# Kernel tuning notes

Hardware: AMD Instinct MI355X
Metric: run time of the kernel (lower is better)

## Reference

```python
import jax, jax.numpy as jnp
import numpy as np

EPS = 1e-8
NUM_LAYERS = 6


def setup_inputs() -> dict:
    key = jax.random.key(0)
    ks = jax.random.split(key, 8)
    N, Cin, Cout, S, H, W = 4, 256, 256, 512, 64, 64
    fan_in = Cin  # kaiming for 1x1 conv, leaky_relu a=0 -> gain sqrt(2)
    return {
        "x": jax.random.normal(ks[0], (N, Cin, H, W), dtype=jnp.float32),
        "y": jax.random.normal(ks[1], (N, S), dtype=jnp.float32),
        "ch_conv_w": jax.random.normal(ks[2], (Cout, Cin), dtype=jnp.float32) / np.sqrt(fan_in),
        "ch_conv_b": jnp.zeros((Cout,), dtype=jnp.float32),
        "affine_w": jax.random.normal(ks[3], (NUM_LAYERS, Cout, S), dtype=jnp.float32) / np.sqrt(S),
        "affine_b": jnp.zeros((NUM_LAYERS, Cout), dtype=jnp.float32),
        "mod_w": jax.random.normal(ks[4], (NUM_LAYERS, Cout, Cout), dtype=jnp.float32) * np.sqrt(2.0 / Cout),
    }


def _forward(x, y, ch_conv_w, ch_conv_b, affine_w, affine_b, mod_w):
    # 1x1 channel conv (with bias)
    x = jnp.einsum("oi,bihw->bohw", ch_conv_w, x) + ch_conv_b[None, :, None, None]
    x = jnp.repeat(jnp.repeat(x, 2, axis=2), 2, axis=3)
    # channel repeat_interleave(2) -> [N, 2C, H, W]
    x = jnp.repeat(x, 2, axis=1)

    C = x.shape[1] // 2
    for i in range(NUM_LAYERS):
        x1, x2 = x[:, :C], x[:, C:]
        # SpatialShift2d with default directions pads [1,1,1,1] (replicate) then
        # crops the identical region for every split -> exact identity.
        y1 = x1 + x2
        # g-branch: Conv2dMod(k=1) with per-sample style modulation + exact GELU
        s = jnp.einsum("cs,bs->bc", affine_w[i], y) + affine_b[i]  # [B, C]
        wmod = mod_w[i][None] * (s[:, :, None] + 1.0)              # [B, O, I] (style scales OUTPUT channel)
        d = jax.lax.rsqrt(jnp.sum(wmod * wmod, axis=2, keepdims=True) + EPS)
        wmod = wmod * d
        h = jnp.einsum("boi,bihw->bohw", wmod, y1)
        y2 = x2 + jax.nn.gelu(h, approximate=False)
        x = jnp.concatenate([y1, y2], axis=1)

    x1, x2 = x[:, :C], x[:, C:]
    return (x1 + x2) * 0.5


def reference(x, y, ch_conv_w, ch_conv_b, affine_w, affine_b, mod_w):
    return _forward(x, y, ch_conv_w, ch_conv_b, affine_w, affine_b, mod_w)
```

## Files before the change

kernel.cpp:

```cpp
#include <hip/hip_runtime.h>
#include <math.h>

#define NB 4
#define CC 256
#define SS 512
#define NL 6
#define SLOT_HW 65536
#define G_OFF_HW   (7*SLOT_HW)

typedef __attribute__((ext_vector_type(8))) short s16x8;
typedef __attribute__((ext_vector_type(4))) float f32x4;
typedef __attribute__((ext_vector_type(2))) float f32x2;

#define PIN(v) asm volatile("" :: "v"(v))

__device__ __forceinline__ unsigned short f2bf(float f) {
    unsigned u = __builtin_bit_cast(unsigned, f);
    u += 0x7FFFu + ((u >> 16) & 1u);
    return (unsigned short)(u >> 16);
}
__device__ __forceinline__ unsigned cvt_pk_bf16(float lo, float hi) {
    unsigned r;
    asm("v_cvt_pk_bf16_f32 %0, %1, %2" : "=v"(r) : "v"(lo), "v"(hi));
    return r;
}
__device__ __forceinline__ float gelu_fast(float x) {
    float u = x * (1.0f + 0.044715f * x * x);
    float e = __expf(-1.5957691216f * u);
    return x * __builtin_amdgcn_rcpf(1.0f + e);
}


__global__ __launch_bounds__(256) void prep_kernel(
    const float* __restrict__ y, const float* __restrict__ aw,
    const float* __restrict__ ab, const float* __restrict__ mw,
    const float* __restrict__ cw, unsigned short* __restrict__ wsBF)
{
    int w = threadIdx.x >> 6, lane = threadIdx.x & 63;
    float* gtab = (float*)(wsBF + G_OFF_HW);

    if (blockIdx.x < 448) {
        int row = blockIdx.x*4 + w;
        int sl  = row >> 8, m = row & 255;
        const float* src = (sl == 0) ? (cw + (size_t)m*CC)
                                     : (mw + ((size_t)(sl-1)*CC + m)*CC);
        unsigned short* dst = wsBF + (size_t)sl*SLOT_HW;
#pragma unroll
        for (int u = 0; u < 4; ++u) {
            int k = lane + 64*u;
            int f = (m >> 4)*8 + (k >> 5);
            int hw = f*512 + ((k >> 3) & 3)*128 + (m & 15)*8 + (k & 7);
            dst[hw] = f2bf(src[k]);
        }
        return;
    }

    int r  = (blockIdx.x - 448)*4 + w;
    int pl = r >> 8, po = r & 255;

    const float* awr = aw + (size_t)(pl*CC + po)*SS;
    float s[4] = {0.f, 0.f, 0.f, 0.f};
#pragma unroll
    for (int j = 0; j < 8; ++j) {
        int idx = lane + 64*j;
        float a = awr[idx];
#pragma unroll
        for (int b = 0; b < 4; ++b) s[b] += a * y[(size_t)b*SS + idx];
    }
    const float* mwr = mw + ((size_t)pl*CC + po)*CC;
    float qs = 0.f;
#pragma unroll
    for (int u = 0; u < 4; ++u) { float v = mwr[lane + 64*u]; qs += v*v; }
#pragma unroll
    for (int off = 32; off; off >>= 1) {
#pragma unroll
        for (int b = 0; b < 4; ++b) s[b] += __shfl_xor(s[b], off);
        qs += __shfl_xor(qs, off);
    }
    float abv = ab[pl*CC + po];
    if (lane < 4) {
        float t = s[lane] + abv + 1.0f;
        gtab[pl*1024 + lane*256 + po] = t * (1.0f / sqrtf(t*t*qs + 1e-8f));
    }
}

#define BFRAGL(buf, kq, nt, kcl) \
    (lds + (buf)*16384 + ((((kq)*2 + (nt))*2 + (kcl)))*1024)

__global__ __launch_bounds__(512, 4) void fused_kernel(
    const float* __restrict__ x, const float* __restrict__ cb,
    const unsigned short* __restrict__ wsBF, float* __restrict__ out)
{
    __shared__ __align__(16) unsigned char lds[69632];
    float* xS = (float*)(lds + 32768);
    float* S2 = (float*)(lds + 32768);
    const float* gtab = (const float*)(wsBF + G_OFF_HW);

    const int tid  = threadIdx.x;
    const int lane = tid & 63;
    const int w    = tid >> 6;
    const int l15  = lane & 15;
    const int q    = lane >> 4;

    const int bswz  = blockIdx.x & 7;
    const int b     = bswz >> 1;
    const int half  = bswz & 1;
    const int strip = blockIdx.x >> 3;
    const int n0    = strip * 64 + half * 32;

    float y1[2][2][4], y2[2][2][4];
    f32x4 acc[2][2];

#pragma unroll
    for (int t = 0; t < 2; ++t)
#pragma unroll
        for (int s = 0; s < 2; ++s) acc[t][s] = 0;

    float4 xr[4];
#pragma unroll
    for (int p = 0; p < 4; ++p) {
        int row = (tid >> 3) + 64*p, c4 = (tid & 7) * 4;
        xr[p] = *(const float4*)&x[((size_t)(b*CC + row))*4096 + n0 + c4];
    }
    s16x8 aS[8][2];
#pragma unroll
    for (int p = 0; p < 4; ++p)
#pragma unroll
    for (int t = 0; t < 2; ++t)
        aS[p][t] = *(const s16x8*)(wsBF + (size_t)(((2*w+t)*8 + p)*512) + lane*8);

#pragma unroll
    for (int p = 0; p < 4; ++p) {
        int row = (tid >> 3) + 64*p, c4 = (tid & 7) * 4;
        *(float4*)&xS[row*36 + c4] = xr[p];
    }
    __syncthreads();
    {
        int n = tid & 31, k0 = (tid >> 5) * 16;
        int nt = n >> 4, n15 = n & 15;
#pragma unroll
        for (int j = 0; j < 4; ++j) {
            int k = k0 + 4*j;
            float v0 = xS[(k+0)*36 + n], v1 = xS[(k+1)*36 + n];
            float v2 = xS[(k+2)*36 + n], v3 = xS[(k+3)*36 + n];
            uint2 hv; hv.x = cvt_pk_bf16(v0, v1); hv.y = cvt_pk_bf16(v2, v3);
            int kq = k >> 6, kcl = (k >> 5) & 1, qq = (k >> 3) & 3, jb = k & 7;
            *(uint2*)(BFRAGL(0,kq,nt,kcl) + (16*qq + n15)*16 + jb*2) = hv;
        }
    }
#pragma unroll
    for (int p = 0; p < 4; ++p) { PIN(aS[p][0]); PIN(aS[p][1]); }
    __syncthreads();
    {
        const unsigned short* slot = wsBF;
        __builtin_amdgcn_s_setprio(1);
#pragma unroll
        for (int step = 0; step < 8; ++step) {
            if (step < 4) {
#pragma unroll
                for (int t = 0; t < 2; ++t)
                    aS[step+4][t] = *(const s16x8*)(slot + (size_t)(((2*w+t)*8 + step+4)*512) + lane*8);
            }
            int kq = step >> 1, kcl = step & 1;
#pragma unroll
            for (int s = 0; s < 2; ++s) {
                s16x8 bh = *(const s16x8*)(BFRAGL(0,kq,s,kcl) + lane*16);
#pragma unroll
                for (int t = 0; t < 2; ++t)
                    acc[t][s] = __builtin_amdgcn_mfma_f32_16x16x32_bf16(aS[step][t], bh, acc[t][s], 0, 0, 0);
            }
        }
        __builtin_amdgcn_s_setprio(0);
    }

#pragma unroll
    for (int t = 0; t < 2; ++t)
#pragma unroll
    for (int s = 0; s < 2; ++s)
#pragma unroll
    for (int r = 0; r < 4; ++r) {
        int m  = 32*w + 16*t + 4*q + r;
        int nl = 16*s + l15;
        S2[m*33 + nl] = acc[t][s][r] + cb[m];
    }
    __syncthreads();
#pragma unroll
    for (int t = 0; t < 2; ++t)
#pragma unroll
    for (int s = 0; s < 2; ++s)
#pragma unroll
    for (int r = 0; r < 4; ++r) {
        int c  = 32*w + 16*t + 4*q + r;
        int nl = 16*s + l15;
        float a  = S2[(c >> 1)*33 + nl];
        float bb = S2[(128 + (c >> 1))*33 + nl];
        y1[t][s][r] = a + bb;
        y2[t][s][r] = bb;
    }

    for (int l = 0; l < NL; ++l) {
        const int buf = l & 1;
        const unsigned short* slot = wsBF + (size_t)(1 + l)*SLOT_HW;
#pragma unroll
        for (int t = 0; t < 2; ++t)
#pragma unroll
            for (int s = 0; s < 2; ++s) acc[t][s] = 0;

#pragma unroll
        for (int p = 0; p < 4; ++p)
#pragma unroll
        for (int t = 0; t < 2; ++t)
            aS[p][t] = *(const s16x8*)(slot + (size_t)(((2*w+t)*8 + p)*512) + lane*8);
        float4 gv[2];
#pragma unroll
        for (int t = 0; t < 2; ++t)
            gv[t] = *(const float4*)&gtab[l*1024 + b*256 + 32*w + 16*t + 4*q];

        {
            int kq = w >> 1, kcl = w & 1, jb = 4*(q & 1);
#pragma unroll
            for (int t = 0; t < 2; ++t) {
                int qq = 2*t + (q >> 1);
#pragma unroll
                for (int s = 0; s < 2; ++s) {
                    uint2 hv;
                    hv.x = cvt_pk_bf16(y1[t][s][0], y1[t][s][1]);
                    hv.y = cvt_pk_bf16(y1[t][s][2], y1[t][s][3]);
                    *(uint2*)(BFRAGL(buf,kq,s,kcl) + (16*qq + l15)*16 + jb*2) = hv;
                }
            }
        }
#pragma unroll
        for (int p = 0; p < 4; ++p) { PIN(aS[p][0]); PIN(aS[p][1]); }
        __syncthreads();
        __builtin_amdgcn_s_setprio(1);
#pragma unroll
        for (int step = 0; step < 8; ++step) {
            if (step < 4) {
#pragma unroll
                for (int t = 0; t < 2; ++t)
                    aS[step+4][t] = *(const s16x8*)(slot + (size_t)(((2*w+t)*8 + step+4)*512) + lane*8);
            }
            int kq = step >> 1, kcl = step & 1;
#pragma unroll
            for (int s = 0; s < 2; ++s) {
                s16x8 bh = *(const s16x8*)(BFRAGL(buf,kq,s,kcl) + lane*16);
#pragma unroll
                for (int t = 0; t < 2; ++t)
                    acc[t][s] = __builtin_amdgcn_mfma_f32_16x16x32_bf16(aS[step][t], bh, acc[t][s], 0, 0, 0);
            }
        }
        __builtin_amdgcn_s_setprio(0);

        if (l < NL - 1) {
#pragma unroll
            for (int t = 0; t < 2; ++t)
#pragma unroll
            for (int s = 0; s < 2; ++s)
#pragma unroll
            for (int r = 0; r < 4; ++r) {
                y2[t][s][r] += gelu_fast(acc[t][s][r] * gv[t][r]);
                y1[t][s][r] += y2[t][s][r];
            }
        } else {
#pragma unroll
            for (int t = 0; t < 2; ++t)
#pragma unroll
            for (int s = 0; s < 2; ++s)
#pragma unroll
            for (int r = 0; r < 4; ++r) {
                float yf = y2[t][s][r] + gelu_fast(acc[t][s][r] * gv[t][r]);
                float v  = 0.5f*(y1[t][s][r] + yf);
                int ch  = 32*w + 16*t + 4*q + r;
                int wpx = half*32 + 16*s + l15;
                f32x2 vv = {v, v};
                size_t base = (((size_t)(b*CC + ch)*128 + 2*strip))*128 + 2*wpx;
                __builtin_nontemporal_store(vv, (f32x2*)&out[base]);
                __builtin_nontemporal_store(vv, (f32x2*)&out[base + 128]);
            }
        }
    }
}

extern "C" void kernel_launch(void* const* d_in, const int* in_sizes, int n_in,
                              void* d_out, int out_size, void* d_ws, size_t ws_size,
                              hipStream_t stream) {
    const float* x  = (const float*)d_in[0];
    const float* y  = (const float*)d_in[1];
    const float* cw = (const float*)d_in[2];
    const float* cb = (const float*)d_in[3];
    const float* aw = (const float*)d_in[4];
    const float* ab = (const float*)d_in[5];
    const float* mw = (const float*)d_in[6];
    float* out = (float*)d_out;

    unsigned short* wsBF = (unsigned short*)d_ws;

    prep_kernel<<<832, 256, 0, stream>>>(y, aw, ab, mw, cw, wsBF);
    fused_kernel<<<512, 512, 0, stream>>>(x, cb, wsBF, out);
}
```

Measured before the change: 120.2 us.

## Halve per-block pixel tile to 16 and double grid for higher occupancy

Each block now handles 16 pixels instead of 32, so the grid doubles to 1024 blocks and LDS drops to 40KB. The launch-bounds occupancy hint rises from 4 to 8. The A-fragment prefetch becomes a 3-deep ring buffer of weight registers, which cuts register pressure. The gtab load moves after the MFMA loop, and the bias loads are vectorised. The aim is more resident waves to hide the latency of the global weight loads. In exchange, every weight fragment is loaded twice as often across the grid, and each B fragment read feeds only two MFMAs.

```diff
diff --git a/kernel.cpp b/kernel.cpp
--- a/kernel.cpp
+++ b/kernel.cpp
@@ -84,16 +84,16 @@
     }
 }
 
-#define BFRAGL(buf, kq, nt, kcl) \
-    (lds + (buf)*16384 + ((((kq)*2 + (nt))*2 + (kcl)))*1024)
-
-__global__ __launch_bounds__(512, 4) void fused_kernel(
+#define BFRAG16(buf, kq, kcl) \
+    (lds + (buf)*8192 + ((kq)*2 + (kcl))*1024)
+
+__global__ __launch_bounds__(512, 8) void fused_kernel(
     const float* __restrict__ x, const float* __restrict__ cb,
     const unsigned short* __restrict__ wsBF, float* __restrict__ out)
 {
-    __shared__ __align__(16) unsigned char lds[69632];
-    float* xS = (float*)(lds + 32768);
-    float* S2 = (float*)(lds + 32768);
+    __shared__ __align__(16) unsigned char lds[40960];
+    float* xS = (float*)(lds + 16384);
+    float* S2 = (float*)(lds + 16384);
     const float* gtab = (const float*)(wsBF + G_OFF_HW);
 
     const int tid  = threadIdx.x;
@@ -102,177 +102,149 @@
     const int l15  = lane & 15;
     const int q    = lane >> 4;
 
-    const int bswz  = blockIdx.x & 7;
-    const int b     = bswz >> 1;
-    const int half  = bswz & 1;
-    const int strip = blockIdx.x >> 3;
-    const int n0    = strip * 64 + half * 32;
-
-    float y1[2][2][4], y2[2][2][4];
-    f32x4 acc[2][2];
-
+    const int b       = blockIdx.x & 3;
+    const int quarter = (blockIdx.x >> 2) & 3;
+    const int strip   = blockIdx.x >> 4;
+    const int n0      = strip*64 + quarter*16;
+
+    float y1[2][4], y2[2][4];
+    f32x4 acc[2];
+    acc[0] = 0; acc[1] = 0;
+
+    float4 xr[2];
+#pragma unroll
+    for (int p = 0; p < 2; ++p) {
+        int row = (tid >> 2) + 128*p, c4 = (tid & 3) * 4;
+        xr[p] = *(const float4*)&x[((size_t)(b*CC + row))*4096 + n0 + c4];
+    }
+    s16x8 aA[3][2];
+#pragma unroll
+    for (int p = 0; p < 2; ++p)
 #pragma unroll
     for (int t = 0; t < 2; ++t)
-#pragma unroll
-        for (int s = 0; s < 2; ++s) acc[t][s] = 0;
-
-    float4 xr[4];
-#pragma unroll
-    for (int p = 0; p < 4; ++p) {
-        int row = (tid >> 3) + 64*p, c4 = (tid & 7) * 4;
-        xr[p] = *(const float4*)&x[((size_t)(b*CC + row))*4096 + n0 + c4];
-    }
-    s16x8 aS[8][2];
-#pragma unroll
-    for (int p = 0; p < 4; ++p)
-#pragma unroll
-    for (int t = 0; t < 2; ++t)
-        aS[p][t] = *(const s16x8*)(wsBF + (size_t)(((2*w+t)*8 + p)*512) + lane*8);
-
-#pragma unroll
-    for (int p = 0; p < 4; ++p) {
-        int row = (tid >> 3) + 64*p, c4 = (tid & 7) * 4;
-        *(float4*)&xS[row*36 + c4] = xr[p];
+        aA[p][t] = *(const s16x8*)(wsBF + (size_t)(((2*w+t)*8 + p)*512) + lane*8);
+
+#pragma unroll
+    for (int p = 0; p < 2; ++p) {
+        int row = (tid >> 2) + 128*p, c4 = (tid & 3) * 4;
+        *(float4*)&xS[row*24 + c4] = xr[p];
     }
     __syncthreads();
     {
-        int n = tid & 31, k0 = (tid >> 5) * 16;
-        int nt = n >> 4, n15 = n & 15;
-#pragma unroll
-        for (int j = 0; j < 4; ++j) {
-            int k = k0 + 4*j;
-            float v0 = xS[(k+0)*36 + n], v1 = xS[(k+1)*36 + n];
-            float v2 = xS[(k+2)*36 + n], v3 = xS[(k+3)*36 + n];
-            uint2 hv; hv.x = cvt_pk_bf16(v0, v1); hv.y = cvt_pk_bf16(v2, v3);
-            int kq = k >> 6, kcl = (k >> 5) & 1, qq = (k >> 3) & 3, jb = k & 7;
-            *(uint2*)(BFRAGL(0,kq,nt,kcl) + (16*qq + n15)*16 + jb*2) = hv;
-        }
-    }
-#pragma unroll
-    for (int p = 0; p < 4; ++p) { PIN(aS[p][0]); PIN(aS[p][1]); }
+        int n = tid & 15, k0 = (tid >> 4) * 8;
+        float v[8];
+#pragma unroll
+        for (int i = 0; i < 8; ++i) v[i] = xS[(k0+i)*24 + n];
+        uint4 hv;
+        hv.x = cvt_pk_bf16(v[0], v[1]); hv.y = cvt_pk_bf16(v[2], v[3]);
+        hv.z = cvt_pk_bf16(v[4], v[5]); hv.w = cvt_pk_bf16(v[6], v[7]);
+        int kq = k0 >> 6, kcl = (k0 >> 5) & 1, qq = (k0 >> 3) & 3;
+        *(uint4*)(BFRAG16(0,kq,kcl) + (16*qq + n)*16) = hv;
+    }
+    PIN(aA[0][0]); PIN(aA[0][1]); PIN(aA[1][0]); PIN(aA[1][1]);
     __syncthreads();
     {
         const unsigned short* slot = wsBF;
         __builtin_amdgcn_s_setprio(1);
 #pragma unroll
         for (int step = 0; step < 8; ++step) {
-            if (step < 4) {
+            if (step < 6) {
 #pragma unroll
                 for (int t = 0; t < 2; ++t)
-                    aS[step+4][t] = *(const s16x8*)(slot + (size_t)(((2*w+t)*8 + step+4)*512) + lane*8);
-            }
-            int kq = step >> 1, kcl = step & 1;
-#pragma unroll
-            for (int s = 0; s < 2; ++s) {
-                s16x8 bh = *(const s16x8*)(BFRAGL(0,kq,s,kcl) + lane*16);
-#pragma unroll
-                for (int t = 0; t < 2; ++t)
-                    acc[t][s] = __builtin_amdgcn_mfma_f32_16x16x32_bf16(aS[step][t], bh, acc[t][s], 0, 0, 0);
-            }
+                    aA[(step+2)%3][t] = *(const s16x8*)(slot + (size_t)(((2*w+t)*8 + step+2)*512) + lane*8);
+            }
+            s16x8 bh = *(const s16x8*)(BFRAG16(0, step>>1, step&1) + lane*16);
+            acc[0] = __builtin_amdgcn_mfma_f32_16x16x32_bf16(aA[step%3][0], bh, acc[0], 0, 0, 0);
+            acc[1] = __builtin_amdgcn_mfma_f32_16x16x32_bf16(aA[step%3][1], bh, acc[1], 0, 0, 0);
         }
         __builtin_amdgcn_s_setprio(0);
     }
 
+    {
+        float4 cbv[2];
+#pragma unroll
+        for (int t = 0; t < 2; ++t)
+            cbv[t] = *(const float4*)&cb[32*w + 16*t + 4*q];
+#pragma unroll
+        for (int t = 0; t < 2; ++t)
+#pragma unroll
+        for (int r = 0; r < 4; ++r) {
+            int m = 32*w + 16*t + 4*q + r;
+            S2[m*18 + l15] = acc[t][r] + cbv[t][r];
+        }
+    }
+    __syncthreads();
 #pragma unroll
     for (int t = 0; t < 2; ++t)
 #pragma unroll
-    for (int s = 0; s < 2; ++s)
-#pragma unroll
     for (int r = 0; r < 4; ++r) {
-        int m  = 32*w + 16*t + 4*q + r;
-        int nl = 16*s + l15;
-        S2[m*33 + nl] = acc[t][s][r] + cb[m];
-    }
-    __syncthreads();
-#pragma unroll
-    for (int t = 0; t < 2; ++t)
-#pragma unroll
-    for (int s = 0; s < 2; ++s)
-#pragma unroll
-    for (int r = 0; r < 4; ++r) {
-        int c  = 32*w + 16*t + 4*q + r;
-        int nl = 16*s + l15;
-        float a  = S2[(c >> 1)*33 + nl];
-        float bb = S2[(128 + (c >> 1))*33 + nl];
-        y1[t][s][r] = a + bb;
-        y2[t][s][r] = bb;
+        int c = 32*w + 16*t + 4*q + r, h = c >> 1;
+        float a  = S2[h*18 + l15];
+        float bb = S2[(128 + h)*18 + l15];
+        y1[t][r] = a + bb;
+        y2[t][r] = bb;
     }
 
     for (int l = 0; l < NL; ++l) {
         const int buf = l & 1;
         const unsigned short* slot = wsBF + (size_t)(1 + l)*SLOT_HW;
-#pragma unroll
-        for (int t = 0; t < 2; ++t)
-#pragma unroll
-            for (int s = 0; s < 2; ++s) acc[t][s] = 0;
-
-#pragma unroll
-        for (int p = 0; p < 4; ++p)
-#pragma unroll
-        for (int t = 0; t < 2; ++t)
-            aS[p][t] = *(const s16x8*)(slot + (size_t)(((2*w+t)*8 + p)*512) + lane*8);
-        float4 gv[2];
-#pragma unroll
-        for (int t = 0; t < 2; ++t)
-            gv[t] = *(const float4*)&gtab[l*1024 + b*256 + 32*w + 16*t + 4*q];
+        acc[0] = 0; acc[1] = 0;
+
+#pragma unroll
+        for (int p = 0; p < 2; ++p)
+#pragma unroll
+        for (int t = 0; t < 2; ++t)
+            aA[p][t] = *(const s16x8*)(slot + (size_t)(((2*w+t)*8 + p)*512) + lane*8);
 
         {
             int kq = w >> 1, kcl = w & 1, jb = 4*(q & 1);
 #pragma unroll
             for (int t = 0; t < 2; ++t) {
                 int qq = 2*t + (q >> 1);
-#pragma unroll
-                for (int s = 0; s < 2; ++s) {
-                    uint2 hv;
-                    hv.x = cvt_pk_bf16(y1[t][s][0], y1[t][s][1]);
-                    hv.y = cvt_pk_bf16(y1[t][s][2], y1[t][s][3]);
-                    *(uint2*)(BFRAGL(buf,kq,s,kcl) + (16*qq + l15)*16 + jb*2) = hv;
-                }
-            }
-        }
-#pragma unroll
-        for (int p = 0; p < 4; ++p) { PIN(aS[p][0]); PIN(aS[p][1]); }
+                uint2 hv;
+                hv.x = cvt_pk_bf16(y1[t][0], y1[t][1]);
+                hv.y = cvt_pk_bf16(y1[t][2], y1[t][3]);
+                *(uint2*)(BFRAG16(buf,kq,kcl) + (16*qq + l15)*16 + jb*2) = hv;
+            }
+        }
+        PIN(aA[0][0]); PIN(aA[0][1]); PIN(aA[1][0]); PIN(aA[1][1]);
         __syncthreads();
         __builtin_amdgcn_s_setprio(1);
 #pragma unroll
         for (int step = 0; step < 8; ++step) {
-            if (step < 4) {
+            if (step < 6) {
 #pragma unroll
                 for (int t = 0; t < 2; ++t)
-                    aS[step+4][t] = *(const s16x8*)(slot + (size_t)(((2*w+t)*8 + step+4)*512) + lane*8);
-            }
-            int kq = step >> 1, kcl = step & 1;
-#pragma unroll
-            for (int s = 0; s < 2; ++s) {
-                s16x8 bh = *(const s16x8*)(BFRAGL(buf,kq,s,kcl) + lane*16);
-#pragma unroll
-                for (int t = 0; t < 2; ++t)
-                    acc[t][s] = __builtin_amdgcn_mfma_f32_16x16x32_bf16(aS[step][t], bh, acc[t][s], 0, 0, 0);
-            }
+                    aA[(step+2)%3][t] = *(const s16x8*)(slot + (size_t)(((2*w+t)*8 + step+2)*512) + lane*8);
+            }
+            s16x8 bh = *(const s16x8*)(BFRAG16(buf, step>>1, step&1) + lane*16);
+            acc[0] = __builtin_amdgcn_mfma_f32_16x16x32_bf16(aA[step%3][0], bh, acc[0], 0, 0, 0);
+            acc[1] = __builtin_amdgcn_mfma_f32_16x16x32_bf16(aA[step%3][1], bh, acc[1], 0, 0, 0);
         }
         __builtin_amdgcn_s_setprio(0);
 
+        float4 gv[2];
+#pragma unroll
+        for (int t = 0; t < 2; ++t)
+            gv[t] = *(const float4*)&gtab[l*1024 + b*256 + 32*w + 16*t + 4*q];
+
         if (l < NL - 1) {
 #pragma unroll
             for (int t = 0; t < 2; ++t)
 #pragma unroll
-            for (int s = 0; s < 2; ++s)
-#pragma unroll
             for (int r = 0; r < 4; ++r) {
-                y2[t][s][r] += gelu_fast(acc[t][s][r] * gv[t][r]);
-                y1[t][s][r] += y2[t][s][r];
+                y2[t][r] += gelu_fast(acc[t][r] * gv[t][r]);
+                y1[t][r] += y2[t][r];
             }
         } else {
 #pragma unroll
             for (int t = 0; t < 2; ++t)
 #pragma unroll
-            for (int s = 0; s < 2; ++s)
-#pragma unroll
             for (int r = 0; r < 4; ++r) {
-                float yf = y2[t][s][r] + gelu_fast(acc[t][s][r] * gv[t][r]);
-                float v  = 0.5f*(y1[t][s][r] + yf);
+                float yf = y2[t][r] + gelu_fast(acc[t][r] * gv[t][r]);
+                float v  = 0.5f*(y1[t][r] + yf);
                 int ch  = 32*w + 16*t + 4*q + r;
-                int wpx = half*32 + 16*s + l15;
+                int wpx = quarter*16 + l15;
                 f32x2 vv = {v, v};
                 size_t base = (((size_t)(b*CC + ch)*128 + 2*strip))*128 + 2*wpx;
                 __builtin_nontemporal_store(vv, (f32x2*)&out[base]);
@@ -297,5 +269,5 @@
     unsigned short* wsBF = (unsigned short*)d_ws;
 
     prep_kernel<<<832, 256, 0, stream>>>(y, aw, ab, mw, cw, wsBF);
-    fused_kernel<<<512, 512, 0, stream>>>(x, cb, wsBF, out);
-}
+    fused_kernel<<<1024, 512, 0, stream>>>(x, cb, wsBF, out);
+}
```

Result: slower. 147.3 us (+22.6%).

## Pipeline weight loads with inline-asm vmcnt waits and stage gain table in LDS

Applied to the files above, without the earlier changes.

Replaces the compiler-scheduled weight-fragment loads with inline-asm global loads and explicit s_waitcnt vmcnt counters. Five fragments are issued before the barrier and the rest are streamed in during the MFMA steps, so each step waits only for its own data. The per-layer gain table is staged once into LDS, which removes a global load from each layer. The __syncthreads calls become raw barriers that wait only on LDS traffic (lgkmcnt), so outstanding global loads can cross them. This adds LDS use and relies on hand-counted vmcnt values, which could break if the compiler inserts other vector memory ops.

```diff
diff --git a/kernel.cpp b/kernel.cpp
--- a/kernel.cpp
+++ b/kernel.cpp
@@ -12,8 +12,6 @@
 typedef __attribute__((ext_vector_type(4))) float f32x4;
 typedef __attribute__((ext_vector_type(2))) float f32x2;
 
-#define PIN(v) asm volatile("" :: "v"(v))
-
 __device__ __forceinline__ unsigned short f2bf(float f) {
     unsigned u = __builtin_bit_cast(unsigned, f);
     u += 0x7FFFu + ((u >> 16) & 1u);
@@ -29,7 +27,11 @@
     float e = __expf(-1.5957691216f * u);
     return x * __builtin_amdgcn_rcpf(1.0f + e);
 }
-
+__device__ __forceinline__ s16x8 aload(const unsigned short* p) {
+    s16x8 r;
+    asm volatile("global_load_dwordx4 %0, %1, off" : "=v"(r) : "v"(p));
+    return r;
+}
 
 __global__ __launch_bounds__(256) void prep_kernel(
     const float* __restrict__ y, const float* __restrict__ aw,
@@ -87,13 +89,40 @@
 #define BFRAGL(buf, kq, nt, kcl) \
     (lds + (buf)*16384 + ((((kq)*2 + (nt))*2 + (kcl)))*1024)
 
+#define ISSUE(p) { \
+    aS[p][0] = aload(slot + (size_t)(((2*w+0)*8 + (p))*512) + lane*8); \
+    aS[p][1] = aload(slot + (size_t)(((2*w+1)*8 + (p))*512) + lane*8); }
+#define WAITA(N, st) asm volatile("s_waitcnt vmcnt(" #N ")" \
+    : "+v"(aS[st][0]), "+v"(aS[st][1]))
+#define STEPX(st) { \
+    s16x8 b0 = *(const s16x8*)(BFRAGL(buf,(st)>>1,0,(st)&1) + lane*16); \
+    s16x8 b1 = *(const s16x8*)(BFRAGL(buf,(st)>>1,1,(st)&1) + lane*16); \
+    acc[0][0] = __builtin_amdgcn_mfma_f32_16x16x32_bf16(aS[st][0], b0, acc[0][0],0,0,0); \
+    acc[1][0] = __builtin_amdgcn_mfma_f32_16x16x32_bf16(aS[st][1], b0, acc[1][0],0,0,0); \
+    acc[0][1] = __builtin_amdgcn_mfma_f32_16x16x32_bf16(aS[st][0], b1, acc[0][1],0,0,0); \
+    acc[1][1] = __builtin_amdgcn_mfma_f32_16x16x32_bf16(aS[st][1], b1, acc[1][1],0,0,0); \
+}
+#define MFMA_PHASE() \
+    ISSUE(5); WAITA(10,0); STEPX(0); \
+    ISSUE(6); WAITA(10,1); STEPX(1); \
+    ISSUE(7); WAITA(10,2); STEPX(2); \
+    WAITA(8,3);  STEPX(3); \
+    WAITA(6,4);  STEPX(4); \
+    WAITA(4,5);  STEPX(5); \
+    WAITA(2,6);  STEPX(6); \
+    WAITA(0,7);  STEPX(7);
+#define RAW_BARRIER() { \
+    asm volatile("s_waitcnt lgkmcnt(0)" ::: "memory"); \
+    __builtin_amdgcn_s_barrier(); }
+
 __global__ __launch_bounds__(512, 4) void fused_kernel(
     const float* __restrict__ x, const float* __restrict__ cb,
     const unsigned short* __restrict__ wsBF, float* __restrict__ out)
 {
-    __shared__ __align__(16) unsigned char lds[69632];
+    __shared__ __align__(16) unsigned char lds[75776];
     float* xS = (float*)(lds + 32768);
     float* S2 = (float*)(lds + 32768);
+    float* gS = (float*)(lds + 69632);
     const float* gtab = (const float*)(wsBF + G_OFF_HW);
 
     const int tid  = threadIdx.x;
@@ -110,66 +139,47 @@
 
     float y1[2][2][4], y2[2][2][4];
     f32x4 acc[2][2];
+    s16x8 aS[8][2];
 
 #pragma unroll
     for (int t = 0; t < 2; ++t)
 #pragma unroll
         for (int s = 0; s < 2; ++s) acc[t][s] = 0;
 
-    float4 xr[4];
+    if (tid < 384) {
+        int gl = tid >> 6, gm = (tid & 63) * 4;
+        float4 gvv = *(const float4*)&gtab[gl*1024 + b*256 + gm];
+        *(float4*)&gS[gl*256 + gm] = gvv;
+    }
 #pragma unroll
     for (int p = 0; p < 4; ++p) {
         int row = (tid >> 3) + 64*p, c4 = (tid & 7) * 4;
-        xr[p] = *(const float4*)&x[((size_t)(b*CC + row))*4096 + n0 + c4];
-    }
-    s16x8 aS[8][2];
-#pragma unroll
-    for (int p = 0; p < 4; ++p)
-#pragma unroll
-    for (int t = 0; t < 2; ++t)
-        aS[p][t] = *(const s16x8*)(wsBF + (size_t)(((2*w+t)*8 + p)*512) + lane*8);
-
-#pragma unroll
-    for (int p = 0; p < 4; ++p) {
-        int row = (tid >> 3) + 64*p, c4 = (tid & 7) * 4;
-        *(float4*)&xS[row*36 + c4] = xr[p];
-    }
-    __syncthreads();
-    {
-        int n = tid & 31, k0 = (tid >> 5) * 16;
-        int nt = n >> 4, n15 = n & 15;
-#pragma unroll
-        for (int j = 0; j < 4; ++j) {
-            int k = k0 + 4*j;
-            float v0 = xS[(k+0)*36 + n], v1 = xS[(k+1)*36 + n];
-            float v2 = xS[(k+2)*36 + n], v3 = xS[(k+3)*36 + n];
-            uint2 hv; hv.x = cvt_pk_bf16(v0, v1); hv.y = cvt_pk_bf16(v2, v3);
-            int kq = k >> 6, kcl = (k >> 5) & 1, qq = (k >> 3) & 3, jb = k & 7;
-            *(uint2*)(BFRAGL(0,kq,nt,kcl) + (16*qq + n15)*16 + jb*2) = hv;
-        }
-    }
-#pragma unroll
-    for (int p = 0; p < 4; ++p) { PIN(aS[p][0]); PIN(aS[p][1]); }
-    __syncthreads();
+        float4 v = *(const float4*)&x[((size_t)(b*CC + row))*4096 + n0 + c4];
+        *(float4*)&xS[row*36 + c4] = v;
+    }
+    asm volatile("" ::: "memory");
     {
         const unsigned short* slot = wsBF;
+#pragma unroll
+        for (int p = 0; p < 5; ++p) ISSUE(p);
+        RAW_BARRIER();
+        {
+            int n = tid & 31, k0 = (tid >> 5) * 16;
+            int nt = n >> 4, n15 = n & 15;
+#pragma unroll
+            for (int j = 0; j < 4; ++j) {
+                int k = k0 + 4*j;
+                float v0 = xS[(k+0)*36 + n], v1 = xS[(k+1)*36 + n];
+                float v2 = xS[(k+2)*36 + n], v3 = xS[(k+3)*36 + n];
+                uint2 hv; hv.x = cvt_pk_bf16(v0, v1); hv.y = cvt_pk_bf16(v2, v3);
+                int kq = k >> 6, kcl = (k >> 5) & 1, qq = (k >> 3) & 3, jb = k & 7;
+                *(uint2*)(BFRAGL(0,kq,nt,kcl) + (16*qq + n15)*16 + jb*2) = hv;
+            }
+        }
+        RAW_BARRIER();
+        const int buf = 0;
         __builtin_amdgcn_s_setprio(1);
-#pragma unroll
-        for (int step = 0; step < 8; ++step) {
-            if (step < 4) {
-#pragma unroll
-                for (int t = 0; t < 2; ++t)
-                    aS[step+4][t] = *(const s16x8*)(slot + (size_t)(((2*w+t)*8 + step+4)*512) + lane*8);
-            }
-            int kq = step >> 1, kcl = step & 1;
-#pragma unroll
-            for (int s = 0; s < 2; ++s) {
-                s16x8 bh = *(const s16x8*)(BFRAGL(0,kq,s,kcl) + lane*16);
-#pragma unroll
-                for (int t = 0; t < 2; ++t)
-                    acc[t][s] = __builtin_amdgcn_mfma_f32_16x16x32_bf16(aS[step][t], bh, acc[t][s], 0, 0, 0);
-            }
-        }
+        MFMA_PHASE();
         __builtin_amdgcn_s_setprio(0);
     }
 
@@ -206,15 +216,9 @@
 #pragma unroll
             for (int s = 0; s < 2; ++s) acc[t][s] = 0;
 
-#pragma unroll
-        for (int p = 0; p < 4; ++p)
-#pragma unroll
-        for (int t = 0; t < 2; ++t)
-            aS[p][t] = *(const s16x8*)(slot + (size_t)(((2*w+t)*8 + p)*512) + lane*8);
-        float4 gv[2];
-#pragma unroll
-        for (int t = 0; t < 2; ++t)
-            gv[t] = *(const float4*)&gtab[l*1024 + b*256 + 32*w + 16*t + 4*q];
+        asm volatile("" ::: "memory");
+#pragma unroll
+        for (int p = 0; p < 5; ++p) ISSUE(p);
 
         {
             int kq = w >> 1, kcl = w & 1, jb = 4*(q & 1);
@@ -230,27 +234,15 @@
                 }
             }
         }
-#pragma unroll
-        for (int p = 0; p < 4; ++p) { PIN(aS[p][0]); PIN(aS[p][1]); }
-        __syncthreads();
+        RAW_BARRIER();
         __builtin_amdgcn_s_setprio(1);
-#pragma unroll
-        for (int step = 0; step < 8; ++step) {
-            if (step < 4) {
-#pragma unroll
-                for (int t = 0; t < 2; ++t)
-                    aS[step+4][t] = *(const s16x8*)(slot + (size_t)(((2*w+t)*8 + step+4)*512) + lane*8);
-            }
-            int kq = step >> 1, kcl = step & 1;
-#pragma unroll
-            for (int s = 0; s < 2; ++s) {
-                s16x8 bh = *(const s16x8*)(BFRAGL(buf,kq,s,kcl) + lane*16);
-#pragma unroll
-                for (int t = 0; t < 2; ++t)
-                    acc[t][s] = __builtin_amdgcn_mfma_f32_16x16x32_bf16(aS[step][t], bh, acc[t][s], 0, 0, 0);
-            }
-        }
+        MFMA_PHASE();
         __builtin_amdgcn_s_setprio(0);
+
+        float4 gv[2];
+#pragma unroll
+        for (int t = 0; t < 2; ++t)
+            gv[t] = *(const float4*)&gS[l*256 + 32*w + 16*t + 4*q];
 
         if (l < NL - 1) {
 #pragma unroll
```

Measured after the change: 119.6 us, median of 2. Within noise of the previous version (-0.5%).
